# Kernel tuning notes

Measured on AMD Instinct MI355X. Metric: run time of the kernel, lower is better.

## Reference

```python
import jax, jax.numpy as jnp
import numpy as np

N_SPECIES = 2
N_RBF = 16
HIDDEN = 64
CUTOFF = 2.5


def setup_inputs() -> dict:
    key = jax.random.key(0)
    ks = jax.random.split(key, 10)
    B, N = 8, 1024
    positions = jax.random.uniform(ks[0], (B, N, 3), dtype=jnp.float32) * 10.0
    types = jax.random.randint(ks[1], (B, N), 0, N_SPECIES)
    in_dim = N_SPECIES + N_SPECIES * N_RBF  # 34
    def lin(k, fan_in, fan_out):
        bound = 1.0 / np.sqrt(fan_in)
        kw, kb = jax.random.split(k)
        W = jax.random.uniform(kw, (fan_in, fan_out), minval=-bound, maxval=bound, dtype=jnp.float32)
        b = jax.random.uniform(kb, (fan_out,), minval=-bound, maxval=bound, dtype=jnp.float32)
        return W, b
    W1, b1 = lin(ks[2], in_dim, 64)
    W2, b2 = lin(ks[3], 64, 64)
    W3, b3 = lin(ks[4], 64, HIDDEN)
    return {"positions": positions, "types": types,
            "W1": W1, "b1": b1, "W2": W2, "b2": b2, "W3": W3, "b3": b3}


def _forward(positions, types, W1, b1, W2, b2, W3, b3):
    B, N, _ = positions.shape
    # pairwise distances with safe sqrt (zero grad on diagonal, matching torch norm subgradient)
    disp = positions[:, :, None, :] - positions[:, None, :, :]          # [B,N,N,3]
    sq = jnp.sum(disp * disp, axis=-1)                                   # [B,N,N]
    nz = sq > 0.0
    d = jnp.sqrt(jnp.where(nz, sq, 1.0)) * nz
    # RBF expansion
    centers = jnp.linspace(0.0, CUTOFF, N_RBF)
    widths = jnp.full((N_RBF,), CUTOFF / max(N_RBF - 1, 1))
    diff = d[..., None] - centers                                        # [B,N,N,R]
    rbf = jnp.exp(-(diff ** 2) / (widths ** 2 + 1e-12))
    # smooth polynomial cutoff
    x = d / CUTOFF
    cut = jnp.where(d < CUTOFF, 1.0 - 6.0 * x ** 5 + 15.0 * x ** 4 - 10.0 * x ** 3, 0.0)
    rbf = rbf * cut[..., None]
    eye = jnp.eye(N, dtype=bool)[None, :, :, None]
    rbf = jnp.where(eye, 0.0, rbf)
    # species-weighted neighbor aggregation
    onehot = jax.nn.one_hot(types, N_SPECIES, dtype=positions.dtype)      # [B,N,S]
    env = jnp.einsum('bijr,bjs->birs', rbf, onehot).reshape(B, N, -1)     # [B,N,R*S]
    feats = jnp.concatenate([onehot, env], axis=-1)                       # [B,N,S+S*R]
    h = jax.nn.silu(feats @ W1 + b1)
    h = jax.nn.silu(h @ W2 + b2)
    return h @ W3 + b3                                                    # [B,N,HIDDEN]


def reference(positions, types, W1, b1, W2, b2, W3, b3):
    return _forward(positions, types, W1, b1, W2, b2, W3, b3)
```

## Files before the change

### kernel.cpp

```cpp
#include <hip/hip_runtime.h>
#include <hip/hip_bf16.h>

#define NTHREADS 256
#define N_ATOMS 1024
#define HIDDEN 64

__global__ __launch_bounds__(NTHREADS) void LocalFeatureEncoder_40063454937486_kernel(
    const float* __restrict__ pos,
    const int*   __restrict__ types,
    const float* __restrict__ W1,
    const float* __restrict__ b1,
    const float* __restrict__ W2,
    const float* __restrict__ b2,
    const float* __restrict__ W3,
    const float* __restrict__ b3,
    float*       __restrict__ out)
{
    const int a    = blockIdx.x;
    const int bidx = a >> 10;
    const int i    = a & (N_ATOMS - 1);
    const int tid  = threadIdx.x;
    const int lane = tid & 63;
    const int wav  = tid >> 6;

    __shared__ float qd [N_ATOMS];
    __shared__ float qm0[N_ATOMS];
    __shared__ float qm1[N_ATOMS];
    __shared__ float partial[4 * 32];
    __shared__ float feats[64];
    __shared__ float h1s[64];
    __shared__ int   cnt;

    const float* pf   = pos + (size_t)bidx * (N_ATOMS * 3);
    const int*   typb = types + (size_t)bidx * N_ATOMS;

    const float4 p0 = *(const float4*)(pf + tid * 12);
    const float4 p1 = *(const float4*)(pf + tid * 12 + 4);
    const float4 p2 = *(const float4*)(pf + tid * 12 + 8);
    const int4   tv = *(const int4*)(typb + tid * 4);

    const float xi = pf[i * 3 + 0];
    const float yi = pf[i * 3 + 1];
    const float zi = pf[i * 3 + 2];

    if (tid == 0) cnt = 0;
    __syncthreads();

    {
        const float px[4] = {p0.x, p0.w, p1.z, p2.y};
        const float py[4] = {p0.y, p1.x, p1.w, p2.z};
        const float pz[4] = {p0.z, p1.y, p2.x, p2.w};
        const int   tj[4] = {tv.x, tv.y, tv.z, tv.w};

#pragma unroll
        for (int q = 0; q < 4; ++q) {
            const int j = tid * 4 + q;
            const float dx = xi - px[q], dy = yi - py[q], dz = zi - pz[q];
            const float sq = dx * dx + dy * dy + dz * dz;
            const bool pred = (j != i) && (sq < 6.25f);

            const unsigned long long mask = __ballot(pred);
            int base = 0;
            if (lane == 0 && mask) base = atomicAdd(&cnt, (int)__popcll(mask));
            base = __shfl(base, 0, 64);
            if (pred) {
                const float d  = sqrtf(sq);
                const float x  = d * 0.4f;
                const float x3 = x * x * x;
                const float cutv = 1.0f + x3 * (-10.0f + x * (15.0f - 6.0f * x));
                const int idx = base + (int)__popcll(mask & ((1ull << lane) - 1ull));
                qd [idx] = d;
                qm0[idx] = (tj[q] == 0) ? cutv : 0.0f;
                qm1[idx] = (tj[q] == 0) ? 0.0f : cutv;
            }
        }
    }
    __syncthreads();
    const int n = cnt;

    {
        const int p = tid >> 5;
        const int f = tid & 31;
        const int r = f >> 1;
        const int s = f & 1;
        const float c = (float)r * (2.5f / 15.0f);
        const float inv_w2 = 36.0f;
        const float* __restrict__ qm = (s == 0) ? qm0 : qm1;

        float acc = 0.0f;
        for (int e = p; e < n; e += 8) {
            const float d    = qd[e];
            const float m    = qm[e];
            const float diff = d - c;
            acc += m * __expf(-(diff * diff) * inv_w2);
        }
        acc += __shfl_xor(acc, 32, 64);
        if (lane < 32) partial[wav * 32 + f] = acc;
        if (tid == 0) {
            const int ti = typb[i];
            feats[0] = (ti == 0) ? 1.0f : 0.0f;
            feats[1] = (ti == 1) ? 1.0f : 0.0f;
        }
    }
    __syncthreads();
    if (tid < 32)
        feats[2 + tid] = partial[tid] + partial[32 + tid] + partial[64 + tid] + partial[96 + tid];
    __syncthreads();

    if (tid < HIDDEN) {
        float h = b1[tid];
#pragma unroll
        for (int k = 0; k < 34; k++) h += feats[k] * W1[k * HIDDEN + tid];
        h = h / (1.0f + __expf(-h));
        h1s[tid] = h;
    }
    __syncthreads();
    if (tid < HIDDEN) {
        float h = b2[tid];
#pragma unroll
        for (int k = 0; k < HIDDEN; k++) h += h1s[k] * W2[k * HIDDEN + tid];
        h = h / (1.0f + __expf(-h));
        feats[tid] = h;
    }
    __syncthreads();
    if (tid < HIDDEN) {
        float o = b3[tid];
#pragma unroll
        for (int k = 0; k < HIDDEN; k++) o += feats[k] * W3[k * HIDDEN + tid];
        out[(size_t)a * HIDDEN + tid] = o;
    }
}

extern "C" void kernel_launch(void* const* d_in, const int* in_sizes, int n_in,
                              void* d_out, int out_size, void* d_ws, size_t ws_size,
                              hipStream_t stream) {
    const float* pos   = (const float*)d_in[0];
    const int*   types = (const int*)d_in[1];
    const float* W1    = (const float*)d_in[2];
    const float* b1    = (const float*)d_in[3];
    const float* W2    = (const float*)d_in[4];
    const float* b2    = (const float*)d_in[5];
    const float* W3    = (const float*)d_in[6];
    const float* b3    = (const float*)d_in[7];
    float*       out   = (float*)d_out;

    const int BN = in_sizes[1];

    LocalFeatureEncoder_40063454937486_kernel<<<BN, NTHREADS, 0, stream>>>(
        pos, types, W1, b1, W2, b2, W3, b3, out);
}
```

Before: 89.88 us.

## Share exp across species via signed mask and fuse MLP into one wave

Encodes the neighbor species as the sign of the stored cutoff weight, so each RBF exponential is computed once and split into two species accumulators, halving exp work. Compaction now uses one atomic per wave instead of four. The three MLP layers run in wave 0 with wave barriers instead of block-wide syncs. This relies on LDS ordering within a wave being correct under wave_barrier.

```diff
diff --git a/kernel.cpp b/kernel.cpp
--- a/kernel.cpp
+++ b/kernel.cpp
@@ -1,5 +1,4 @@
 #include <hip/hip_runtime.h>
-#include <hip/hip_bf16.h>
 
 #define NTHREADS 256
 #define N_ATOMS 1024
@@ -24,8 +23,7 @@
     const int wav  = tid >> 6;
 
     __shared__ float qd [N_ATOMS];
-    __shared__ float qm0[N_ATOMS];
-    __shared__ float qm1[N_ATOMS];
+    __shared__ float qm [N_ATOMS];
     __shared__ float partial[4 * 32];
     __shared__ float feats[64];
     __shared__ float h1s[64];
@@ -52,50 +50,63 @@
         const float pz[4] = {p0.z, p1.y, p2.x, p2.w};
         const int   tj[4] = {tv.x, tv.y, tv.z, tv.w};
 
+        float sq[4];
+        bool  pr[4];
+        unsigned long long m[4];
 #pragma unroll
         for (int q = 0; q < 4; ++q) {
             const int j = tid * 4 + q;
             const float dx = xi - px[q], dy = yi - py[q], dz = zi - pz[q];
-            const float sq = dx * dx + dy * dy + dz * dz;
-            const bool pred = (j != i) && (sq < 6.25f);
+            sq[q] = dx * dx + dy * dy + dz * dz;
+            pr[q] = (j != i) && (sq[q] < 6.25f);
+            m[q]  = __ballot(pr[q]);
+        }
 
-            const unsigned long long mask = __ballot(pred);
-            int base = 0;
-            if (lane == 0 && mask) base = atomicAdd(&cnt, (int)__popcll(mask));
-            base = __shfl(base, 0, 64);
-            if (pred) {
-                const float d  = sqrtf(sq);
+        const int tot = (int)(__popcll(m[0]) + __popcll(m[1]) +
+                              __popcll(m[2]) + __popcll(m[3]));
+        int base = 0;
+        if (lane == 0 && tot) base = atomicAdd(&cnt, tot);
+        base = __shfl(base, 0, 64);
+
+        const unsigned long long lt = (1ull << lane) - 1ull;
+        int off = base;
+#pragma unroll
+        for (int q = 0; q < 4; ++q) {
+            if (pr[q]) {
+                const float d  = sqrtf(sq[q]);
                 const float x  = d * 0.4f;
                 const float x3 = x * x * x;
                 const float cutv = 1.0f + x3 * (-10.0f + x * (15.0f - 6.0f * x));
-                const int idx = base + (int)__popcll(mask & ((1ull << lane) - 1ull));
-                qd [idx] = d;
-                qm0[idx] = (tj[q] == 0) ? cutv : 0.0f;
-                qm1[idx] = (tj[q] == 0) ? 0.0f : cutv;
+                const int idx = off + (int)__popcll(m[q] & lt);
+                qd[idx] = d;
+                qm[idx] = (tj[q] == 0) ? cutv : -cutv;
             }
+            off += (int)__popcll(m[q]);
         }
     }
     __syncthreads();
     const int n = cnt;
 
     {
-        const int p = tid >> 5;
-        const int f = tid & 31;
-        const int r = f >> 1;
-        const int s = f & 1;
-        const float c = (float)r * (2.5f / 15.0f);
-        const float inv_w2 = 36.0f;
-        const float* __restrict__ qm = (s == 0) ? qm0 : qm1;
+        const int slot = tid >> 4;
+        const int r    = tid & 15;
+        const float c  = (float)r * (2.5f / 15.0f);
 
-        float acc = 0.0f;
-        for (int e = p; e < n; e += 8) {
+        float a0 = 0.0f, a1 = 0.0f;
+        for (int e = slot; e < n; e += 16) {
             const float d    = qd[e];
-            const float m    = qm[e];
+            const float mm   = qm[e];
             const float diff = d - c;
-            acc += m * __expf(-(diff * diff) * inv_w2);
+            const float ex   = __expf(-(diff * diff) * 36.0f);
+            a0 = fmaf(fmaxf( mm, 0.0f), ex, a0);
+            a1 = fmaf(fmaxf(-mm, 0.0f), ex, a1);
         }
-        acc += __shfl_xor(acc, 32, 64);
-        if (lane < 32) partial[wav * 32 + f] = acc;
+        a0 += __shfl_xor(a0, 16, 64);  a0 += __shfl_xor(a0, 32, 64);
+        a1 += __shfl_xor(a1, 16, 64);  a1 += __shfl_xor(a1, 32, 64);
+        if (lane < 16) {
+            partial[wav * 32 + 2 * r]     = a0;
+            partial[wav * 32 + 2 * r + 1] = a1;
+        }
         if (tid == 0) {
             const int ti = typb[i];
             feats[0] = (ti == 0) ? 1.0f : 0.0f;
@@ -103,30 +114,30 @@
         }
     }
     __syncthreads();
-    if (tid < 32)
-        feats[2 + tid] = partial[tid] + partial[32 + tid] + partial[64 + tid] + partial[96 + tid];
-    __syncthreads();
 
     if (tid < HIDDEN) {
+        if (tid < 32)
+            feats[2 + tid] = partial[tid] + partial[32 + tid] +
+                             partial[64 + tid] + partial[96 + tid];
+        __builtin_amdgcn_wave_barrier();
+
         float h = b1[tid];
 #pragma unroll
-        for (int k = 0; k < 34; k++) h += feats[k] * W1[k * HIDDEN + tid];
+        for (int k = 0; k < 34; k++) h = fmaf(feats[k], W1[k * HIDDEN + tid], h);
         h = h / (1.0f + __expf(-h));
         h1s[tid] = h;
-    }
-    __syncthreads();
-    if (tid < HIDDEN) {
-        float h = b2[tid];
+        __builtin_amdgcn_wave_barrier();
+
+        float g = b2[tid];
 #pragma unroll
-        for (int k = 0; k < HIDDEN; k++) h += h1s[k] * W2[k * HIDDEN + tid];
-        h = h / (1.0f + __expf(-h));
-        feats[tid] = h;
-    }
-    __syncthreads();
-    if (tid < HIDDEN) {
+        for (int k = 0; k < HIDDEN; k++) g = fmaf(h1s[k], W2[k * HIDDEN + tid], g);
+        g = g / (1.0f + __expf(-g));
+        feats[tid] = g;
+        __builtin_amdgcn_wave_barrier();
+
         float o = b3[tid];
 #pragma unroll
-        for (int k = 0; k < HIDDEN; k++) o += feats[k] * W3[k * HIDDEN + tid];
+        for (int k = 0; k < HIDDEN; k++) o = fmaf(feats[k], W3[k * HIDDEN + tid], o);
         out[(size_t)a * HIDDEN + tid] = o;
     }
 }
```

New measurement: 85.12 us. -5.3%, faster.
